# Kernel optimization log

Measured on AMD Instinct MI355X. Metric: run time of the kernel, lower is better.

## Reference

```python
import jax, jax.numpy as jnp
import numpy as np

B, S, D, U = 16, 1024, 1024, 512  # batch, seq, d_model, cfc_units
LN_EPS = 1e-5


def setup_inputs() -> dict:
    key = jax.random.key(0)
    ks = jax.random.split(key, 12)
    sd_in = 1.0 / np.sqrt(D)
    sd_u = 1.0 / np.sqrt(U)
    return {
        "x": jax.random.normal(ks[0], (B, S, D), dtype=jnp.float32),
        "ln_gamma": jnp.ones((D,), jnp.float32),
        "ln_beta": jnp.zeros((D,), jnp.float32),
        # input_proj: Linear(D -> U)
        "w_in": jax.random.uniform(ks[1], (U, D), jnp.float32, -sd_in, sd_in),
        "b_in": jax.random.uniform(ks[2], (U,), jnp.float32, -sd_in, sd_in),
        # GRU weights (PyTorch layout: [3U, U], gate order r, z, n)
        "w_ih": jax.random.uniform(ks[3], (3 * U, U), jnp.float32, -sd_u, sd_u),
        "w_hh": jax.random.uniform(ks[4], (3 * U, U), jnp.float32, -sd_u, sd_u),
        "b_ih": jax.random.uniform(ks[5], (3 * U,), jnp.float32, -sd_u, sd_u),
        "b_hh": jax.random.uniform(ks[6], (3 * U,), jnp.float32, -sd_u, sd_u),
        # output_proj: Linear(U -> D)
        "w_out": jax.random.uniform(ks[7], (D, U), jnp.float32, -sd_u, sd_u),
        "b_out": jax.random.uniform(ks[8], (D,), jnp.float32, -sd_u, sd_u),
    }


def _layernorm(x, gamma, beta):
    mu = jnp.mean(x, axis=-1, keepdims=True)
    var = jnp.mean(jnp.square(x - mu), axis=-1, keepdims=True)
    return (x - mu) * jax.lax.rsqrt(var + LN_EPS) * gamma + beta


def reference(x, ln_gamma, ln_beta, w_in, b_in, w_ih, w_hh, b_ih, b_hh, w_out, b_out):
    residual = x
    xn = _layernorm(x, ln_gamma, ln_beta)                       # [B,S,D]
    u = jnp.einsum("bsd,ud->bsu", xn, w_in) + b_in              # [B,S,U]
    # precompute input-side gate activations for all timesteps (one big GEMM)
    gx = jnp.einsum("bsu,gu->bsg", u, w_ih) + b_ih              # [B,S,3U]

    def step(h, gx_t):                                          # gx_t [B,3U]
        gh = h @ w_hh.T + b_hh                                  # [B,3U]
        xr, xz, xn_ = jnp.split(gx_t, 3, axis=-1)
        hr, hz, hn = jnp.split(gh, 3, axis=-1)
        r = jax.nn.sigmoid(xr + hr)
        z = jax.nn.sigmoid(xz + hz)
        n = jnp.tanh(xn_ + r * hn)
        h_new = (1.0 - z) * n + z * h
        return h_new, h_new

    h0 = jnp.zeros((x.shape[0], w_hh.shape[1]), dtype=jnp.float32)
    h_last, ys = jax.lax.scan(step, h0, jnp.swapaxes(gx, 0, 1))  # ys [S,B,U]
    y = jnp.swapaxes(ys, 0, 1)                                   # [B,S,U]
    out = residual + (jnp.einsum("bsu,du->bsd", y, w_out) + b_out)
    return out, h_last
```

## Files before the change

### kernel.cpp

```cpp
#include <hip/hip_runtime.h>

typedef unsigned short ushort_t;
typedef unsigned int uint_t;
typedef __attribute__((ext_vector_type(8))) short bf16x8;
typedef __attribute__((ext_vector_type(4))) float f32x4;
typedef __attribute__((ext_vector_type(4))) unsigned int uintx4;

#define B_  16
#define S_  1024
#define D_  1024
#define U_  512
#define GU_ 1536

__device__ __forceinline__ ushort_t f2bf(float f) {
  union { float f; uint_t u; } v; v.f = f;
  uint_t r = v.u + 0x7fffu + ((v.u >> 16) & 1u);
  return (ushort_t)(r >> 16);
}
__device__ __forceinline__ float bf2f(ushort_t b) {
  union { uint_t u; float f; } v; v.u = ((uint_t)b) << 16; return v.f;
}

__device__ __forceinline__ int rp16(int m) {
  return ((m & 1023) << 4) | (m >> 10);
}

__global__ void cvt_f32_bf16(const float4* __restrict__ in, ushort4* __restrict__ out, int n4) {
  int i = blockIdx.x * blockDim.x + threadIdx.x;
  int stride = gridDim.x * blockDim.x;
  for (; i < n4; i += stride) {
    float4 f = in[i];
    ushort4 o; o.x = f2bf(f.x); o.y = f2bf(f.y); o.z = f2bf(f.z); o.w = f2bf(f.w);
    out[i] = o;
  }
}

__global__ __launch_bounds__(256) void ln_kernel(
    const float* __restrict__ x, const float* __restrict__ gamma,
    const float* __restrict__ beta, ushort_t* __restrict__ xn)
{
  int row = blockIdx.x;
  int t = threadIdx.x;
  const float* xr = x + (size_t)row * 1024;
  float4 v = *(const float4*)(xr + t * 4);
  float s = v.x + v.y + v.z + v.w;
  float ss = v.x * v.x + v.y * v.y + v.z * v.z + v.w * v.w;
#pragma unroll
  for (int o = 32; o > 0; o >>= 1) {
    s  += __shfl_down(s, o, 64);
    ss += __shfl_down(ss, o, 64);
  }
  __shared__ float red[2][4];
  __shared__ float mv[2];
  int wv = t >> 6, ln = t & 63;
  if (ln == 0) { red[0][wv] = s; red[1][wv] = ss; }
  __syncthreads();
  if (t == 0) {
    float S1 = red[0][0] + red[0][1] + red[0][2] + red[0][3];
    float S2 = red[1][0] + red[1][1] + red[1][2] + red[1][3];
    float mu = S1 * (1.f / 1024.f);
    float var = S2 * (1.f / 1024.f) - mu * mu;
    mv[0] = mu;
    mv[1] = rsqrtf(var + 1e-5f);
  }
  __syncthreads();
  float mu = mv[0], rs = mv[1];
  float4 gm = *(const float4*)(gamma + t * 4);
  float4 bt = *(const float4*)(beta + t * 4);
  ushort4 o;
  o.x = f2bf((v.x - mu) * rs * gm.x + bt.x);
  o.y = f2bf((v.y - mu) * rs * gm.y + bt.y);
  o.z = f2bf((v.z - mu) * rs * gm.z + bt.z);
  o.w = f2bf((v.w - mu) * rs * gm.w + bt.w);
  *(ushort4*)(xn + (size_t)row * 1024 + t * 4) = o;
}

template<int RES, int OBF, int APERM, int CPERM>
__global__ __launch_bounds__(256, 2) void gemm_bt(
    const ushort_t* __restrict__ A, const ushort_t* __restrict__ Bw,
    const float* __restrict__ bias, const float* __restrict__ resid,
    void* __restrict__ Cout, int M, int N, int K)
{
  __shared__ ushort_t As[128][40];
  __shared__ ushort_t Bs[128][40];
  int bm = blockIdx.x, bn = blockIdx.y;
  int tid = threadIdx.x;
  int wave = tid >> 6, lane = tid & 63;
  int wm = wave >> 1, wn = wave & 1;
  int q = lane >> 4, l16 = lane & 15;
  f32x4 acc[4][4];
#pragma unroll
  for (int i = 0; i < 4; i++)
#pragma unroll
    for (int j = 0; j < 4; j++) acc[i][j] = (f32x4){0.f, 0.f, 0.f, 0.f};
  int r0 = tid >> 2, kc = tid & 3;
  const int nk = K >> 5;
  for (int it = 0; it < nk; ++it) {
#pragma unroll
    for (int h = 0; h < 2; ++h) {
      int r = r0 + h * 64;
      int arow = bm * 128 + r;
      if (APERM) arow = rp16(arow);
      const uint4* pa = (const uint4*)(A + (size_t)arow * K + it * 32 + kc * 8);
      *(uint4*)&As[r][kc * 8] = *pa;
      const uint4* pb = (const uint4*)(Bw + (size_t)(bn * 128 + r) * K + it * 32 + kc * 8);
      *(uint4*)&Bs[r][kc * 8] = *pb;
    }
    __syncthreads();
    bf16x8 af[4], bfr[4];
#pragma unroll
    for (int i = 0; i < 4; i++) af[i]  = *(bf16x8*)&As[wm * 64 + i * 16 + l16][q * 8];
#pragma unroll
    for (int j = 0; j < 4; j++) bfr[j] = *(bf16x8*)&Bs[wn * 64 + j * 16 + l16][q * 8];
#pragma unroll
    for (int i = 0; i < 4; i++)
#pragma unroll
      for (int j = 0; j < 4; j++)
        acc[i][j] = __builtin_amdgcn_mfma_f32_16x16x32_bf16(af[i], bfr[j], acc[i][j], 0, 0, 0);
    __syncthreads();
  }
#pragma unroll
  for (int i = 0; i < 4; i++) {
#pragma unroll
    for (int j = 0; j < 4; j++) {
      int n = bn * 128 + wn * 64 + j * 16 + l16;
      float bv = bias[n];
#pragma unroll
      for (int rr = 0; rr < 4; rr++) {
        int m = bm * 128 + wm * 64 + i * 16 + q * 4 + rr;
        float v = acc[i][j][rr] + bv;
        if (RES) v += resid[(size_t)m * N + n];
        int cm = CPERM ? rp16(m) : m;
        if (OBF) ((ushort_t*)Cout)[(size_t)cm * N + n] = f2bf(v);
        else     ((float*)Cout)[(size_t)cm * N + n] = v;
      }
    }
  }
}


#define SCAN_KS(ks, n)                                                         \
  {                                                                            \
    asm volatile("s_waitcnt vmcnt(" #n ")" : "+v"(sv[ks]) :: "memory");        \
    bf16x8 hf = *(bf16x8*)&sv[ks];                                             \
    _Pragma("unroll")                                                          \
    for (int gi = 0; gi < 3; ++gi) {                                           \
      bf16x8 wf;                                                               \
      if ((ks) < 8)                                                            \
        wf = *(const bf16x8*)(wlds +                                           \
              (size_t)((gi * 2 + wv) * 8 + ((ks) & 7)) * 512 + lane * 8);      \
      else                                                                     \
        wf = wreg[gi][(ks) & 7];                                               \
      acc[gi] = __builtin_amdgcn_mfma_f32_16x16x32_bf16(hf, wf, acc[gi], 0, 0, 0); \
    }                                                                          \
  }

__global__ __launch_bounds__(128, 1) void scan_kernel(
    const ushort_t* __restrict__ gx, const float* __restrict__ w_hh,
    const float* __restrict__ b_hh, uint_t* __restrict__ mdata,
    uint_t* __restrict__ mtag, ushort_t* __restrict__ y,
    float* __restrict__ h_last)
{
  extern __shared__ char smem[];
  ushort_t* wlds = (ushort_t*)smem;

  const int m = blockIdx.x;
  const int c0 = m * 32;
  const int t = threadIdx.x;
  const int wv = t >> 6, lane = t & 63, q = lane >> 4, l16 = lane & 15;
  const int cl = (wv << 4) + l16;

  for (int idx = t; idx < 48 * 64; idx += 128) {
    int cc = idx >> 6, ln = idx & 63;
    int gi = cc >> 4, wv2 = (cc >> 3) & 1, ks = cc & 7;
    int n = c0 + (wv2 << 4) + (ln & 15);
    int k0 = (ks << 5) + ((ln >> 4) << 3);
    const float* src = w_hh + (size_t)(gi * 512 + n) * 512 + k0;
    float4 f0 = *(const float4*)src;
    float4 f1 = *(const float4*)(src + 4);
    uint4 pk;
    pk.x = (uint_t)f2bf(f0.x) | ((uint_t)f2bf(f0.y) << 16);
    pk.y = (uint_t)f2bf(f0.z) | ((uint_t)f2bf(f0.w) << 16);
    pk.z = (uint_t)f2bf(f1.x) | ((uint_t)f2bf(f1.y) << 16);
    pk.w = (uint_t)f2bf(f1.z) | ((uint_t)f2bf(f1.w) << 16);
    *(uint4*)(wlds + (size_t)cc * 512 + ln * 8) = pk;
  }
  bf16x8 wreg[3][8];
#pragma unroll
  for (int gi = 0; gi < 3; ++gi)
#pragma unroll
    for (int k8 = 0; k8 < 8; ++k8) {
      const float* src = w_hh + (size_t)(gi * 512 + c0 + cl) * 512 + (8 + k8) * 32 + q * 8;
      float4 f0 = *(const float4*)src;
      float4 f1 = *(const float4*)(src + 4);
      bf16x8 wf;
      wf[0] = (short)f2bf(f0.x); wf[1] = (short)f2bf(f0.y);
      wf[2] = (short)f2bf(f0.z); wf[3] = (short)f2bf(f0.w);
      wf[4] = (short)f2bf(f1.x); wf[5] = (short)f2bf(f1.y);
      wf[6] = (short)f2bf(f1.z); wf[7] = (short)f2bf(f1.w);
      wreg[gi][k8] = wf;
    }

  const float bhr = b_hh[c0 + cl];
  const float bhz = b_hh[512 + c0 + cl];
  const float bhn = b_hh[1024 + c0 + cl];
  float hcur[4] = {0.f, 0.f, 0.f, 0.f};

  __syncthreads();

  for (int step = 0; step < S_; ++step) {
    ushort_t gxv[3][4];
#pragma unroll
    for (int g = 0; g < 3; ++g)
#pragma unroll
      for (int r = 0; r < 4; ++r)
        gxv[g][r] = gx[(size_t)(step * 16 + (q << 2) + r) * GU_ + g * 512 + c0 + cl];

    f32x4 acc[3] = {{0.f,0.f,0.f,0.f},{0.f,0.f,0.f,0.f},{0.f,0.f,0.f,0.f}};

    if (step > 0) {
      const uint_t want = (uint_t)step;
      const int slot = (step - 1) & 1;
      const uint_t* tp = mtag + slot * 16 + (lane & 15);
      uint_t tv;
      do {
        asm volatile("global_load_dword %0, %1, off sc0 sc1"
                     : "=v"(tv) : "v"(tp) : "memory");
        asm volatile("s_waitcnt vmcnt(0)" ::: "memory");
      } while (!__all((int)(tv == want)));
      const uint_t* dbase = mdata + (size_t)slot * 4096 + l16 * 256 + q * 4;
      uintx4 sv[16];
#pragma unroll
      for (int ks = 0; ks < 16; ++ks) {
        const uint_t* p = dbase + ks * 16;
        asm volatile("global_load_dwordx4 %0, %1, off sc0 sc1"
                     : "=&v"(sv[ks]) : "v"(p) : "memory");
      }
      SCAN_KS(0, 15)  SCAN_KS(1, 14)  SCAN_KS(2, 13)  SCAN_KS(3, 12)
      SCAN_KS(4, 11)  SCAN_KS(5, 10)  SCAN_KS(6, 9)   SCAN_KS(7, 8)
      SCAN_KS(8, 7)   SCAN_KS(9, 6)   SCAN_KS(10, 5)  SCAN_KS(11, 4)
      SCAN_KS(12, 3)  SCAN_KS(13, 2)  SCAN_KS(14, 1)  SCAN_KS(15, 0)
    }

    ushort_t hb16[4];
#pragma unroll
    for (int r = 0; r < 4; ++r) {
      float xr  = bf2f(gxv[0][r]);
      float xz  = bf2f(gxv[1][r]);
      float xnn = bf2f(gxv[2][r]);
      float rr = 1.f / (1.f + __expf(-(xr + acc[0][r] + bhr)));
      float zz = 1.f / (1.f + __expf(-(xz + acc[1][r] + bhz)));
      float na = xnn + rr * (acc[2][r] + bhn);
      float ng = 1.f - 2.f / (1.f + __expf(2.f * na));
      float hv = (1.f - zz) * ng + zz * hcur[r];
      hcur[r] = hv;
      hb16[r] = f2bf(hv);
    }

#pragma unroll
    for (int r = 0; r < 4; ++r)
      y[(size_t)(step * 16 + (q << 2) + r) * U_ + c0 + cl] = hb16[r];

    if (step < S_ - 1) {
      const int oslot = step & 1;
#pragma unroll
      for (int r = 0; r < 4; ++r) {
        uint_t other = (uint_t)__shfl_xor((int)(uint_t)hb16[r], 1, 64);
        if ((lane & 1) == 0) {
          uint_t dw = ((uint_t)hb16[r]) | (other << 16);
          int b = (q << 2) + r;
          uint_t* pp = mdata + oslot * 4096 + b * 256 + ((c0 + cl) >> 1);
          asm volatile("global_store_dword %0, %1, off sc0 sc1"
                       :: "v"(pp), "v"(dw) : "memory");
        }
      }
      __syncthreads();
      if (t == 0) {
        uint_t tagv = (uint_t)(step + 1);
        uint_t* tp = mtag + oslot * 16 + m;
        asm volatile("global_store_dword %0, %1, off sc0 sc1"
                     :: "v"(tp), "v"(tagv) : "memory");
      }
    }
  }

#pragma unroll
  for (int r = 0; r < 4; ++r)
    h_last[((q << 2) + r) * 512 + c0 + cl] = hcur[r];
}

extern "C" void kernel_launch(void* const* d_in, const int* in_sizes, int n_in,
                              void* d_out, int out_size, void* d_ws, size_t ws_size,
                              hipStream_t stream) {
  const float* x     = (const float*)d_in[0];
  const float* ln_g  = (const float*)d_in[1];
  const float* ln_b  = (const float*)d_in[2];
  const float* w_in  = (const float*)d_in[3];
  const float* b_in  = (const float*)d_in[4];
  const float* w_ih  = (const float*)d_in[5];
  const float* w_hh  = (const float*)d_in[6];
  const float* b_ih  = (const float*)d_in[7];
  const float* b_hh  = (const float*)d_in[8];
  const float* w_out = (const float*)d_in[9];
  const float* b_out = (const float*)d_in[10];

  float* out = (float*)d_out;
  float* h_last = out + (size_t)B_ * S_ * D_;

  char* ws = (char*)d_ws;
  size_t off = 0;
  ushort_t* xn   = (ushort_t*)(ws + off); off += (size_t)B_ * S_ * D_ * 2;
  ushort_t* u    = (ushort_t*)(ws + off); off += (size_t)B_ * S_ * U_ * 2;
  ushort_t* gx   = (ushort_t*)(ws + off); off += (size_t)B_ * S_ * GU_ * 2;
  ushort_t* y    = (ushort_t*)(ws + off); off += (size_t)B_ * S_ * U_ * 2;
  ushort_t* winb = (ushort_t*)(ws + off); off += (size_t)U_ * D_ * 2;
  ushort_t* wihb = (ushort_t*)(ws + off); off += (size_t)GU_ * U_ * 2;
  uint_t* mtag   = (uint_t*)(ws + off);   off += 256;
  ushort_t* woub = (ushort_t*)(ws + off); off += (size_t)D_ * U_ * 2;
  uint_t* mdata  = (uint_t*)xn;

  cvt_f32_bf16<<<512, 256, 0, stream>>>((const float4*)w_in,  (ushort4*)winb, U_ * D_ / 4);
  cvt_f32_bf16<<<512, 256, 0, stream>>>((const float4*)w_ih,  (ushort4*)wihb, GU_ * U_ / 4);
  cvt_f32_bf16<<<512, 256, 0, stream>>>((const float4*)w_out, (ushort4*)woub, D_ * U_ / 4);

  ln_kernel<<<B_ * S_, 256, 0, stream>>>(x, ln_g, ln_b, xn);

  gemm_bt<0, 1, 0, 0><<<dim3(B_ * S_ / 128, U_ / 128), 256, 0, stream>>>(
      xn, winb, b_in, nullptr, u, B_ * S_, U_, D_);
  gemm_bt<0, 1, 0, 1><<<dim3(B_ * S_ / 128, GU_ / 128), 256, 0, stream>>>(
      u, wihb, b_ih, nullptr, gx, B_ * S_, GU_, U_);

  hipMemsetAsync(mtag, 0, 256, stream);

  (void)hipFuncSetAttribute(reinterpret_cast<const void*>(scan_kernel),
                            hipFuncAttributeMaxDynamicSharedMemorySize, 49152);
  scan_kernel<<<16, 128, 49152, stream>>>(gx, w_hh, b_hh, mdata, mtag, y, h_last);

  gemm_bt<1, 0, 1, 0><<<dim3(B_ * S_ / 128, D_ / 128), 256, 0, stream>>>(
      y, woub, b_out, x, out, B_ * S_, D_, U_);
}
```

Measured before the change: 3.150 ms.

## Embed step tags in hidden-state exchange words to drop per-step block barrier

Each bf16 hidden value is now stored as a 32-bit word carrying the step number in its upper half. Consumers validate the tag per chunk and re-load any stale chunk, so the producer no longer needs a __syncthreads before publishing the block tag. Loads are regrouped into four double-buffered groups that overlap with the MFMAs, and the y store moves after the exchange stores. The exchange traffic doubles in size, and the bounded poll and retry budgets could silently produce wrong results if they are exhausted.

```diff
diff --git a/kernel.cpp b/kernel.cpp
--- a/kernel.cpp
+++ b/kernel.cpp
@@ -139,21 +139,70 @@
 }
 
 
-#define SCAN_KS(ks, n)                                                         \
-  {                                                                            \
-    asm volatile("s_waitcnt vmcnt(" #n ")" : "+v"(sv[ks]) :: "memory");        \
-    bf16x8 hf = *(bf16x8*)&sv[ks];                                             \
-    _Pragma("unroll")                                                          \
-    for (int gi = 0; gi < 3; ++gi) {                                           \
-      bf16x8 wf;                                                               \
-      if ((ks) < 8)                                                            \
-        wf = *(const bf16x8*)(wlds +                                           \
-              (size_t)((gi * 2 + wv) * 8 + ((ks) & 7)) * 512 + lane * 8);      \
-      else                                                                     \
-        wf = wreg[gi][(ks) & 7];                                               \
-      acc[gi] = __builtin_amdgcn_mfma_f32_16x16x32_bf16(hf, wf, acc[gi], 0, 0, 0); \
-    }                                                                          \
-  }
+template<int G>
+__device__ __forceinline__ void issue_g(uintx4 (&sb)[2][4][2], const uint_t* dbase) {
+#pragma unroll
+  for (int s = 0; s < 4; ++s) {
+    asm volatile("global_load_dwordx4 %0, %2, off sc0 sc1\n\t"
+                 "global_load_dwordx4 %1, %2, off offset:16 sc0 sc1"
+                 : "=&v"(sb[G & 1][s][0]), "=&v"(sb[G & 1][s][1])
+                 : "v"(dbase + (G * 4 + s) * 32) : "memory");
+  }
+}
+
+template<int G, int CNT>
+__device__ __forceinline__ void cons_g(uintx4 (&sb)[2][4][2], const uint_t* dbase,
+                                       uint_t want, int& retry_budget,
+                                       const ushort_t* wlds,
+                                       const bf16x8 (&wreg)[3][8],
+                                       int wv, int lane, f32x4 (&acc)[3]) {
+  constexpr int P = G & 1;
+  if constexpr (CNT == 8) {
+    asm volatile("s_waitcnt vmcnt(8)"
+        : "+v"(sb[P][0][0]), "+v"(sb[P][0][1]), "+v"(sb[P][1][0]), "+v"(sb[P][1][1]),
+          "+v"(sb[P][2][0]), "+v"(sb[P][2][1]), "+v"(sb[P][3][0]), "+v"(sb[P][3][1])
+        :: "memory");
+  } else {
+    asm volatile("s_waitcnt vmcnt(0)"
+        : "+v"(sb[P][0][0]), "+v"(sb[P][0][1]), "+v"(sb[P][1][0]), "+v"(sb[P][1][1]),
+          "+v"(sb[P][2][0]), "+v"(sb[P][2][1]), "+v"(sb[P][3][0]), "+v"(sb[P][3][1])
+        :: "memory");
+  }
+#pragma unroll
+  for (int s = 0; s < 4; ++s) {
+    const int ks = G * 4 + s;
+    uint_t bad = 0;
+#pragma unroll
+    for (int d = 0; d < 4; ++d)
+      bad |= ((sb[P][s][0][d] >> 16) ^ want) | ((sb[P][s][1][d] >> 16) ^ want);
+    while (!__all(bad == 0) && --retry_budget >= 0) {
+      asm volatile("global_load_dwordx4 %0, %2, off sc0 sc1\n\t"
+                   "global_load_dwordx4 %1, %2, off offset:16 sc0 sc1"
+                   : "=&v"(sb[P][s][0]), "=&v"(sb[P][s][1])
+                   : "v"(dbase + ks * 32) : "memory");
+      asm volatile("s_waitcnt vmcnt(0)"
+                   : "+v"(sb[P][s][0]), "+v"(sb[P][s][1]) :: "memory");
+      bad = 0;
+#pragma unroll
+      for (int d = 0; d < 4; ++d)
+        bad |= ((sb[P][s][0][d] >> 16) ^ want) | ((sb[P][s][1][d] >> 16) ^ want);
+    }
+    union { bf16x8 h8; uint_t u[4]; } hu;
+    hu.u[0] = __builtin_amdgcn_perm(sb[P][s][0][1], sb[P][s][0][0], 0x05040100u);
+    hu.u[1] = __builtin_amdgcn_perm(sb[P][s][0][3], sb[P][s][0][2], 0x05040100u);
+    hu.u[2] = __builtin_amdgcn_perm(sb[P][s][1][1], sb[P][s][1][0], 0x05040100u);
+    hu.u[3] = __builtin_amdgcn_perm(sb[P][s][1][3], sb[P][s][1][2], 0x05040100u);
+#pragma unroll
+    for (int gi = 0; gi < 3; ++gi) {
+      bf16x8 wf;
+      if (ks < 8)
+        wf = *(const bf16x8*)(wlds + (size_t)((gi * 2 + wv) * 8 + (ks & 7)) * 512 + lane * 8);
+      else
+        wf = wreg[gi][ks & 7];
+      acc[gi] = __builtin_amdgcn_mfma_f32_16x16x32_bf16(hu.h8, wf, acc[gi], 0, 0, 0);
+    }
+  }
+}
 
 __global__ __launch_bounds__(128, 1) void scan_kernel(
     const ushort_t* __restrict__ gx, const float* __restrict__ w_hh,
@@ -208,6 +257,9 @@
 
   __syncthreads();
 
+  int poll_budget  = 1 << 20;
+  int retry_budget = 1 << 16;
+
   for (int step = 0; step < S_; ++step) {
     ushort_t gxv[3][4];
 #pragma unroll
@@ -223,23 +275,23 @@
       const int slot = (step - 1) & 1;
       const uint_t* tp = mtag + slot * 16 + (lane & 15);
       uint_t tv;
-      do {
+      for (;;) {
         asm volatile("global_load_dword %0, %1, off sc0 sc1"
                      : "=v"(tv) : "v"(tp) : "memory");
         asm volatile("s_waitcnt vmcnt(0)" ::: "memory");
-      } while (!__all((int)(tv == want)));
-      const uint_t* dbase = mdata + (size_t)slot * 4096 + l16 * 256 + q * 4;
-      uintx4 sv[16];
-#pragma unroll
-      for (int ks = 0; ks < 16; ++ks) {
-        const uint_t* p = dbase + ks * 16;
-        asm volatile("global_load_dwordx4 %0, %1, off sc0 sc1"
-                     : "=&v"(sv[ks]) : "v"(p) : "memory");
+        if (__all((int)(tv == want))) break;
+        if (--poll_budget < 0) break;
       }
-      SCAN_KS(0, 15)  SCAN_KS(1, 14)  SCAN_KS(2, 13)  SCAN_KS(3, 12)
-      SCAN_KS(4, 11)  SCAN_KS(5, 10)  SCAN_KS(6, 9)   SCAN_KS(7, 8)
-      SCAN_KS(8, 7)   SCAN_KS(9, 6)   SCAN_KS(10, 5)  SCAN_KS(11, 4)
-      SCAN_KS(12, 3)  SCAN_KS(13, 2)  SCAN_KS(14, 1)  SCAN_KS(15, 0)
+      const uint_t* dbase = mdata + (size_t)slot * 8192 + l16 * 512 + q * 8;
+      uintx4 sb[2][4][2];
+      issue_g<0>(sb, dbase);
+      issue_g<1>(sb, dbase);
+      cons_g<0, 8>(sb, dbase, want, retry_budget, wlds, wreg, wv, lane, acc);
+      issue_g<2>(sb, dbase);
+      cons_g<1, 8>(sb, dbase, want, retry_budget, wlds, wreg, wv, lane, acc);
+      issue_g<3>(sb, dbase);
+      cons_g<2, 8>(sb, dbase, want, retry_budget, wlds, wreg, wv, lane, acc);
+      cons_g<3, 0>(sb, dbase, want, retry_budget, wlds, wreg, wv, lane, acc);
     }
 
     ushort_t hb16[4];
@@ -257,31 +309,26 @@
       hb16[r] = f2bf(hv);
     }
 
+    if (step < S_ - 1) {
+      const int oslot = step & 1;
+      const uint_t tag = ((uint_t)(step + 1)) << 16;
+      uint_t* pb = mdata + oslot * 8192 + (c0 + cl);
+#pragma unroll
+      for (int r = 0; r < 4; ++r) {
+        uint_t dw = (uint_t)hb16[r] | tag;
+        asm volatile("global_store_dword %0, %1, off sc0 sc1"
+                     :: "v"(pb + ((q << 2) + r) * 512), "v"(dw) : "memory");
+      }
+      if (t == 0) {
+        uint_t tagv = (uint_t)(step + 1);
+        asm volatile("global_store_dword %0, %1, off sc0 sc1"
+                     :: "v"(mtag + oslot * 16 + m), "v"(tagv) : "memory");
+      }
+    }
+
 #pragma unroll
     for (int r = 0; r < 4; ++r)
       y[(size_t)(step * 16 + (q << 2) + r) * U_ + c0 + cl] = hb16[r];
-
-    if (step < S_ - 1) {
-      const int oslot = step & 1;
-#pragma unroll
-      for (int r = 0; r < 4; ++r) {
-        uint_t other = (uint_t)__shfl_xor((int)(uint_t)hb16[r], 1, 64);
-        if ((lane & 1) == 0) {
-          uint_t dw = ((uint_t)hb16[r]) | (other << 16);
-          int b = (q << 2) + r;
-          uint_t* pp = mdata + oslot * 4096 + b * 256 + ((c0 + cl) >> 1);
-          asm volatile("global_store_dword %0, %1, off sc0 sc1"
-                       :: "v"(pp), "v"(dw) : "memory");
-        }
-      }
-      __syncthreads();
-      if (t == 0) {
-        uint_t tagv = (uint_t)(step + 1);
-        uint_t* tp = mtag + oslot * 16 + m;
-        asm volatile("global_store_dword %0, %1, off sc0 sc1"
-                     :: "v"(tp), "v"(tagv) : "memory");
-      }
-    }
   }
 
 #pragma unroll
@@ -330,6 +377,7 @@
   gemm_bt<0, 1, 0, 1><<<dim3(B_ * S_ / 128, GU_ / 128), 256, 0, stream>>>(
       u, wihb, b_ih, nullptr, gx, B_ * S_, GU_, U_);
 
+  hipMemsetAsync(mdata, 0, 65536, stream);
   hipMemsetAsync(mtag, 0, 256, stream);
 
   (void)hipFuncSetAttribute(reinterpret_cast<const void*>(scan_kernel),
```

Result: slower. 4.771 ms (+51.5%).
